# Performance work log

Hardware: AMD Instinct MI355X
Metric: run time of the kernel (lower is better)

Reference implementation:

```python
import jax, jax.numpy as jnp
import numpy as np

# dims from source: seq_len=784, d_in=2, d_hidden=512, d_out=2, n_layers=3; batch bumped 32->64
T, BS, D_IN, D_H, D_OUT, N_LAYERS = 784, 64, 2, 512, 2, 3


def _glorot(k, shape):
    fan_in, fan_out = shape[-2], shape[-1]
    std = jnp.sqrt(2.0 / (fan_in + fan_out)).astype(jnp.float32)
    return jax.random.normal(k, shape, jnp.float32) * std


def setup_inputs() -> dict:
    key = jax.random.key(0)
    ks = jax.random.split(key, 8)
    x = jax.random.normal(ks[0], (T, BS, D_IN), jnp.float32)
    W0 = _glorot(ks[1], (D_IN, D_H))
    b0 = jnp.zeros((D_H,), jnp.float32)
    # stable_init: uniform in [0.999, 1.001), one diagonal 'a' per layer
    A = jax.random.uniform(ks[2], (N_LAYERS, D_H), jnp.float32, 0.999, 1.001)
    B = _glorot(ks[3], (N_LAYERS, D_H, D_H))  # per-layer input matrix b
    C = _glorot(ks[4], (N_LAYERS, D_H, D_H))  # per-layer output matrix c
    Wf = _glorot(ks[5], (D_H, D_OUT))
    bf = jnp.zeros((D_OUT,), jnp.float32)
    return {"x": x, "W0": W0, "b0": b0, "A": A, "B": B, "C": C, "Wf": Wf, "bf": bf}


def _rnn_layer(x, a, b, c):
    # x: [T, BS, D], diagonal linear recurrence h_t = h_{t-1} * a + x_t @ b; y_t = h_t @ c
    u = jnp.einsum('tbi,ih->tbh', x, b)  # batched GEMM outside the scan

    def step(h, u_t):
        h = h * a + u_t
        return h, h

    h0 = jnp.zeros(u.shape[1:], u.dtype)  # [BS, D_H]
    _, hs = jax.lax.scan(step, h0, u)     # hs: [T, BS, D_H]
    return jnp.einsum('tbh,ho->tbo', hs, c)


def reference(x, W0, b0, A, B, C, Wf, bf):
    # initial Dense + relu
    h = jax.nn.relu(x @ W0 + b0)
    # stacked unidirectional RNN layers, relu after each
    for l in range(A.shape[0]):
        h = jax.nn.relu(_rnn_layer(h, A[l], B[l], C[l]))
    # final Dense (no residual)
    return h @ Wf + bf
```

## Files before the change

### kernel.cpp

```cpp
#include <hip/hip_runtime.h>
#include <hip/hip_bf16.h>

typedef _Float16 f16;
typedef f16 f16x4 __attribute__((ext_vector_type(4)));
typedef f16 f16x8 __attribute__((ext_vector_type(8)));
typedef float f32x4 __attribute__((ext_vector_type(4)));

#define T_LEN 784
#define BATCH 64
#define DH 512
#define NCH (BATCH*DH)
#define M_ROWS (T_LEN*BATCH)
#define NCHUNK 16
#define CLEN 49

#define ACT_SCALE (1.0f/256.0f)
#define ACT_INV   256.0f

#define GLL16(g, s)                                                             \
    __builtin_amdgcn_global_load_lds(                                           \
        (const __attribute__((address_space(1))) void*)(g),                     \
        (__attribute__((address_space(3))) void*)(s), 16, 0, 0)

#define VMCNT(n) asm volatile("s_waitcnt vmcnt(" #n ")" ::: "memory")

__global__ void prep_weights(const float* __restrict__ B, const float* __restrict__ C,
                             f16* __restrict__ Bt, f16* __restrict__ Ct) {
    __shared__ float tile[32][33];
    int z = blockIdx.z;
    const float* src = (z < 3) ? (B + (size_t)z * DH * DH) : (C + (size_t)(z - 3) * DH * DH);
    f16* dst = (z < 3) ? (Bt + (size_t)z * DH * DH) : (Ct + (size_t)(z - 3) * DH * DH);
    int tx = threadIdx.x, ty = threadIdx.y;
    int nb = blockIdx.x * 32, kb = blockIdx.y * 32;
#pragma unroll
    for (int i = 0; i < 4; i++) {
        int k = ty + i * 8;
        tile[k][tx] = src[(size_t)(kb + k) * DH + nb + tx];
    }
    __syncthreads();
#pragma unroll
    for (int i = 0; i < 4; i++) {
        int n = ty + i * 8;
        dst[(size_t)(nb + n) * DH + kb + tx] = (f16)tile[tx][n];
    }
}

__global__ void dense0_kernel(const float* __restrict__ x, const float* __restrict__ W0,
                              const float* __restrict__ b0, f16* __restrict__ H) {
    int tid = blockIdx.x * 256 + threadIdx.x;
    int m = tid >> 6;
    int hb = (tid & 63) * 8;
    float x0 = x[(size_t)m * 2], x1 = x[(size_t)m * 2 + 1];
    f32x4 wa0 = *(const f32x4*)(W0 + hb);
    f32x4 wa1 = *(const f32x4*)(W0 + hb + 4);
    f32x4 wb0 = *(const f32x4*)(W0 + DH + hb);
    f32x4 wb1 = *(const f32x4*)(W0 + DH + hb + 4);
    f32x4 c0 = *(const f32x4*)(b0 + hb);
    f32x4 c1 = *(const f32x4*)(b0 + hb + 4);
    f16x8 o;
#pragma unroll
    for (int j = 0; j < 4; j++) {
        float v = fmaxf(fmaf(x0, wa0[j], fmaf(x1, wb0[j], c0[j])), 0.f) * ACT_SCALE;
        o[j] = (f16)v;
    }
#pragma unroll
    for (int j = 0; j < 4; j++) {
        float v = fmaxf(fmaf(x0, wa1[j], fmaf(x1, wb1[j], c1[j])), 0.f) * ACT_SCALE;
        o[4 + j] = (f16)v;
    }
    *(f16x8*)(H + (size_t)m * DH + hb) = o;
}

template <int RELU>
__global__ __launch_bounds__(256) void gemm_k(const f16* __restrict__ A,
                                              const f16* __restrict__ Bt,
                                              f16* __restrict__ Out) {
    __shared__ __align__(16) f16 As[3][128 * 32];
    __shared__ __align__(16) f16 Bs[3][128 * 32];
    const int tid = threadIdx.x;
    const int lane = tid & 63;
    const int wave = tid >> 6;
    const int wr = wave >> 1, wc = wave & 1;
    const int bid = blockIdx.x;
    const int brow = (bid >> 5) * 8 + (bid & 7);
    const int bcol = (bid >> 3) & 3;
    const size_t mb = (size_t)brow * 128;
    const int nb = bcol * 128;

    const int rl = lane >> 2, sl = lane & 3;
    const int ssl = sl ^ ((rl >> 1) & 3);
    const int rowS0 = wave * 16 + rl;
    const int rowS1 = 64 + wave * 16 + rl;
    const f16* gA0 = A + (mb + rowS0) * DH + ssl * 8;
    const f16* gA1 = A + (mb + rowS1) * DH + ssl * 8;
    const f16* gB0 = Bt + (size_t)(nb + rowS0) * DH + ssl * 8;
    const f16* gB1 = Bt + (size_t)(nb + rowS1) * DH + ssl * 8;
    const int ldsOff0 = (wave * 16) * 32;
    const int ldsOff1 = (64 + wave * 16) * 32;

    const int rA = lane & 15, kq = lane >> 4;
    const int fsl = kq ^ ((rA >> 1) & 3);
    int offA[4], offB[4];
#pragma unroll
    for (int i = 0; i < 4; i++) offA[i] = (wr * 64 + i * 16 + rA) * 32 + fsl * 8;
#pragma unroll
    for (int j = 0; j < 4; j++) offB[j] = (wc * 64 + j * 16 + rA) * 32 + fsl * 8;

    f32x4 acc[4][4] = {};

#define STAGE(b, kt)                        \
    do {                                    \
        GLL16(gA0 + (kt), &As[b][ldsOff0]); \
        GLL16(gA1 + (kt), &As[b][ldsOff1]); \
        GLL16(gB0 + (kt), &Bs[b][ldsOff0]); \
        GLL16(gB1 + (kt), &Bs[b][ldsOff1]); \
    } while (0)

#define COMPUTE(b)                                                                              \
    do {                                                                                        \
        f16x8 af[4], bg[4];                                                                     \
        _Pragma("unroll") for (int i = 0; i < 4; i++) af[i] = *(const f16x8*)&As[b][offA[i]];   \
        _Pragma("unroll") for (int j = 0; j < 4; j++) bg[j] = *(const f16x8*)&Bs[b][offB[j]];   \
        _Pragma("unroll") for (int i = 0; i < 4; i++)                                           \
        _Pragma("unroll") for (int j = 0; j < 4; j++)                                           \
            acc[i][j] = __builtin_amdgcn_mfma_f32_16x16x32_f16(bg[j], af[i], acc[i][j], 0, 0, 0); \
    } while (0)

    STAGE(0, 0);
    STAGE(1, 32);

#pragma unroll
    for (int t = 0; t < 15; ++t) {
        VMCNT(4);
        __builtin_amdgcn_s_barrier();
        if (t < 14) STAGE((t + 2) % 3, (t + 2) * 32);
        COMPUTE(t % 3);
    }
    VMCNT(0);
    __builtin_amdgcn_s_barrier();
    COMPUTE(0);
#undef STAGE
#undef COMPUTE

    const int erow = lane & 15;
    const int ecq = (lane >> 4) * 4;
#pragma unroll
    for (int i = 0; i < 4; i++) {
        size_t row = mb + wr * 64 + i * 16 + erow;
#pragma unroll
        for (int j = 0; j < 4; j++) {
            int col = nb + wc * 64 + j * 16 + ecq;
            f16x4 o;
#pragma unroll
            for (int r = 0; r < 4; r++) {
                float v = acc[i][j][r];
                if (RELU) v = fmaxf(v, 0.f);
                o[r] = (f16)v;
            }
            *(f16x4*)(Out + row * DH + col) = o;
        }
    }
}

__global__ void scan_pass1(const f16* __restrict__ U, const float* __restrict__ Al,
                           float* __restrict__ finals) {
    int tid = blockIdx.x * 256 + threadIdx.x;
    int ch = tid & (NCH - 1);
    int c = tid >> 15;
    float a = Al[ch & (DH - 1)];
    const f16* p = U + (size_t)(c * CLEN) * NCH + ch;
    float h = 0.f;
#pragma unroll
    for (int i = 0; i < CLEN; i++) h = fmaf(h, a, (float)p[(size_t)i * NCH]);
    finals[(size_t)c * NCH + ch] = h;
}

__global__ void scan_pass2(const float* __restrict__ finals, const float* __restrict__ Al,
                           float* __restrict__ carries) {
    int ch = blockIdx.x * 256 + threadIdx.x;
    float a = Al[ch & (DH - 1)];
    float a49 = 1.f;
#pragma unroll
    for (int i = 0; i < CLEN; i++) a49 *= a;
    float carry = 0.f;
#pragma unroll
    for (int c = 0; c < NCHUNK; c++) {
        carries[(size_t)c * NCH + ch] = carry;
        carry = fmaf(carry, a49, finals[(size_t)c * NCH + ch]);
    }
}

__global__ void scan_pass3(f16* __restrict__ U, const float* __restrict__ Al,
                           const float* __restrict__ carries) {
    int tid = blockIdx.x * 256 + threadIdx.x;
    int ch = tid & (NCH - 1);
    int c = tid >> 15;
    float a = Al[ch & (DH - 1)];
    f16* p = U + (size_t)(c * CLEN) * NCH + ch;
    float h = carries[(size_t)c * NCH + ch];
#pragma unroll
    for (int i = 0; i < CLEN; i++) {
        h = fmaf(h, a, (float)p[(size_t)i * NCH]);
        p[(size_t)i * NCH] = (f16)h;
    }
}

__global__ void final_dense(const f16* __restrict__ H, const float* __restrict__ Wf,
                            const float* __restrict__ bf_, float* __restrict__ out) {
    __shared__ float WfS[DH * 2];
    for (int i = threadIdx.x; i < DH * 2; i += 256) WfS[i] = Wf[i];
    __syncthreads();
    int wave = threadIdx.x >> 6, lane = threadIdx.x & 63;
    size_t m = (size_t)blockIdx.x * 4 + wave;
    f16x8 v = *(const f16x8*)(H + m * DH + lane * 8);
    float d0 = 0.f, d1 = 0.f;
#pragma unroll
    for (int j = 0; j < 8; j++) {
        float hv = (float)v[j];
        int h = lane * 8 + j;
        d0 = fmaf(hv, WfS[h * 2], d0);
        d1 = fmaf(hv, WfS[h * 2 + 1], d1);
    }
#pragma unroll
    for (int off = 32; off; off >>= 1) {
        d0 += __shfl_down(d0, off);
        d1 += __shfl_down(d1, off);
    }
    if (lane == 0) {
        out[m * 2] = fmaf(d0, ACT_INV, bf_[0]);
        out[m * 2 + 1] = fmaf(d1, ACT_INV, bf_[1]);
    }
}

extern "C" void kernel_launch(void* const* d_in, const int* in_sizes, int n_in,
                              void* d_out, int out_size, void* d_ws, size_t ws_size,
                              hipStream_t stream) {
    (void)in_sizes; (void)n_in; (void)out_size; (void)ws_size;
    const float* x   = (const float*)d_in[0];
    const float* W0  = (const float*)d_in[1];
    const float* b0  = (const float*)d_in[2];
    const float* A   = (const float*)d_in[3];
    const float* Bw  = (const float*)d_in[4];
    const float* Cw  = (const float*)d_in[5];
    const float* Wf  = (const float*)d_in[6];
    const float* bfv = (const float*)d_in[7];
    float* out = (float*)d_out;

    char* ws = (char*)d_ws;
    size_t off = 0;
    auto alloc = [&](size_t bytes) {
        void* p = ws + off;
        off += (bytes + 255) & ~(size_t)255;
        return p;
    };
    f16* Bt = (f16*)alloc((size_t)3 * DH * DH * 2);
    f16* Ct = (f16*)alloc((size_t)3 * DH * DH * 2);
    f16* P  = (f16*)alloc((size_t)M_ROWS * DH * 2);
    f16* Q  = (f16*)alloc((size_t)M_ROWS * DH * 2);
    float* finals  = (float*)alloc((size_t)NCH * NCHUNK * 4);
    float* carries = (float*)alloc((size_t)NCH * NCHUNK * 4);

    dim3 b256(256);
    prep_weights<<<dim3(16, 16, 6), dim3(32, 8), 0, stream>>>(Bw, Cw, Bt, Ct);
    dense0_kernel<<<M_ROWS * 64 / 256, b256, 0, stream>>>(x, W0, b0, P);
    for (int l = 0; l < 3; l++) {
        const float* Al = A + l * DH;
        gemm_k<0><<<dim3(M_ROWS / 128 * 4), b256, 0, stream>>>(P, Bt + (size_t)l * DH * DH, Q);
        scan_pass1<<<NCH * NCHUNK / 256, b256, 0, stream>>>(Q, Al, finals);
        scan_pass2<<<NCH / 256, b256, 0, stream>>>(finals, Al, carries);
        scan_pass3<<<NCH * NCHUNK / 256, b256, 0, stream>>>(Q, Al, carries);
        gemm_k<1><<<dim3(M_ROWS / 128 * 4), b256, 0, stream>>>(Q, Ct + (size_t)l * DH * DH, P);
    }
    final_dense<<<M_ROWS / 4, b256, 0, stream>>>(P, Wf, bfv, out);
}
```

Before: 379.4 us.

## Widen GEMM block tile to 128x256 with 8 waves per block

```diff
diff --git a/kernel.cpp b/kernel.cpp
--- a/kernel.cpp
+++ b/kernel.cpp
@@ -72,31 +72,27 @@
 }
 
 template <int RELU>
-__global__ __launch_bounds__(256) void gemm_k(const f16* __restrict__ A,
-                                              const f16* __restrict__ Bt,
-                                              f16* __restrict__ Out) {
+__global__ __launch_bounds__(512, 4) void gemm_k(const f16* __restrict__ A,
+                                                 const f16* __restrict__ Bt,
+                                                 f16* __restrict__ Out) {
     __shared__ __align__(16) f16 As[3][128 * 32];
-    __shared__ __align__(16) f16 Bs[3][128 * 32];
+    __shared__ __align__(16) f16 Bs[3][256 * 32];
     const int tid = threadIdx.x;
     const int lane = tid & 63;
     const int wave = tid >> 6;
-    const int wr = wave >> 1, wc = wave & 1;
-    const int bid = blockIdx.x;
-    const int brow = (bid >> 5) * 8 + (bid & 7);
-    const int bcol = (bid >> 3) & 3;
-    const size_t mb = (size_t)brow * 128;
-    const int nb = bcol * 128;
+    const int wr = wave >> 2;
+    const int wc = wave & 3;
+    const size_t mb = (size_t)blockIdx.x * 128;
+    const int nb = blockIdx.y * 256;
 
     const int rl = lane >> 2, sl = lane & 3;
     const int ssl = sl ^ ((rl >> 1) & 3);
-    const int rowS0 = wave * 16 + rl;
-    const int rowS1 = 64 + wave * 16 + rl;
-    const f16* gA0 = A + (mb + rowS0) * DH + ssl * 8;
-    const f16* gA1 = A + (mb + rowS1) * DH + ssl * 8;
-    const f16* gB0 = Bt + (size_t)(nb + rowS0) * DH + ssl * 8;
-    const f16* gB1 = Bt + (size_t)(nb + rowS1) * DH + ssl * 8;
-    const int ldsOff0 = (wave * 16) * 32;
-    const int ldsOff1 = (64 + wave * 16) * 32;
+    const f16* gA  = A  + (mb + wave * 16 + rl) * DH + ssl * 8;
+    const f16* gB0 = Bt + (size_t)(nb + wave * 16 + rl) * DH + ssl * 8;
+    const f16* gB1 = Bt + (size_t)(nb + 128 + wave * 16 + rl) * DH + ssl * 8;
+    const int ldsOffA  = (wave * 16) * 32;
+    const int ldsOffB0 = (wave * 16) * 32;
+    const int ldsOffB1 = (128 + wave * 16) * 32;
 
     const int rA = lane & 15, kq = lane >> 4;
     const int fsl = kq ^ ((rA >> 1) & 3);
@@ -108,12 +104,11 @@
 
     f32x4 acc[4][4] = {};
 
-#define STAGE(b, kt)                        \
-    do {                                    \
-        GLL16(gA0 + (kt), &As[b][ldsOff0]); \
-        GLL16(gA1 + (kt), &As[b][ldsOff1]); \
-        GLL16(gB0 + (kt), &Bs[b][ldsOff0]); \
-        GLL16(gB1 + (kt), &Bs[b][ldsOff1]); \
+#define STAGE(b, kt)                         \
+    do {                                     \
+        GLL16(gA  + (kt), &As[b][ldsOffA]);  \
+        GLL16(gB0 + (kt), &Bs[b][ldsOffB0]); \
+        GLL16(gB1 + (kt), &Bs[b][ldsOffB1]); \
     } while (0)
 
 #define COMPUTE(b)                                                                              \
@@ -131,7 +126,7 @@
 
 #pragma unroll
     for (int t = 0; t < 15; ++t) {
-        VMCNT(4);
+        VMCNT(3);
         __builtin_amdgcn_s_barrier();
         if (t < 14) STAGE((t + 2) % 3, (t + 2) * 32);
         COMPUTE(t % 3);
@@ -261,15 +256,16 @@
     float* carries = (float*)alloc((size_t)NCH * NCHUNK * 4);
 
     dim3 b256(256);
+    dim3 b512(512);
     prep_weights<<<dim3(16, 16, 6), dim3(32, 8), 0, stream>>>(Bw, Cw, Bt, Ct);
     dense0_kernel<<<M_ROWS * 64 / 256, b256, 0, stream>>>(x, W0, b0, P);
     for (int l = 0; l < 3; l++) {
         const float* Al = A + l * DH;
-        gemm_k<0><<<dim3(M_ROWS / 128 * 4), b256, 0, stream>>>(P, Bt + (size_t)l * DH * DH, Q);
+        gemm_k<0><<<dim3(M_ROWS / 128, 2), b512, 0, stream>>>(P, Bt + (size_t)l * DH * DH, Q);
         scan_pass1<<<NCH * NCHUNK / 256, b256, 0, stream>>>(Q, Al, finals);
         scan_pass2<<<NCH / 256, b256, 0, stream>>>(finals, Al, carries);
         scan_pass3<<<NCH * NCHUNK / 256, b256, 0, stream>>>(Q, Al, carries);
-        gemm_k<1><<<dim3(M_ROWS / 128 * 4), b256, 0, stream>>>(Q, Ct + (size_t)l * DH * DH, P);
+        gemm_k<1><<<dim3(M_ROWS / 128, 2), b512, 0, stream>>>(Q, Ct + (size_t)l * DH * DH, P);
     }
     final_dense<<<M_ROWS / 4, b256, 0, stream>>>(P, Wf, bfv, out);
 }
```

Result: slower. 406.8 us (+7.2%).
